# Performance work log

Measured on AMD Instinct MI355X. Metric: run time of the kernel, lower is better.

Reference implementation:

```python
import jax, jax.numpy as jnp
import numpy as np

B, C, T, D = 4, 64, 256, 256   # batch, channel, time, in_feat
H, DK, OUT = 4, 64, 256        # heads, d_k, out_feat
MIN_VALUE = float(np.finfo(np.float32).min)


def _complex_linear(xr, xi, wr, wi, br, bi):
    # ComplexLinear: (fc_r(xr) - fc_i(xi), fc_r(xi) + fc_i(xr))
    out_r = (xr @ wr + br) - (xi @ wi + bi)
    out_i = (xi @ wr + br) + (xr @ wi + bi)
    return out_r, out_i


def setup_inputs() -> dict:
    key = jax.random.key(0)
    ks = jax.random.split(key, 23)
    s = 1.0 / np.sqrt(D)
    inp = {}
    names = ['q_r', 'q_i', 'k_r', 'k_i', 'v_r', 'v_i']
    for i, n in enumerate(names):
        inp[n] = jax.random.normal(ks[i], (B, C, T, D), dtype=jnp.float32)
    inp['mask'] = jnp.ones((B, 1, C), dtype=jnp.int32)
    pi = 6
    for proj in ['q', 'k', 'v', 'o']:
        out_dim = OUT if proj == 'o' else D
        inp[f'w{proj}_r'] = jax.random.normal(ks[pi], (D, out_dim), dtype=jnp.float32) * s; pi += 1
        inp[f'w{proj}_i'] = jax.random.normal(ks[pi], (D, out_dim), dtype=jnp.float32) * s; pi += 1
        inp[f'b{proj}_r'] = jax.random.normal(ks[pi], (out_dim,), dtype=jnp.float32) * 0.01; pi += 1
        inp[f'b{proj}_i'] = jax.random.normal(ks[pi], (out_dim,), dtype=jnp.float32) * 0.01; pi += 1
    return inp


def _split_heads(x):
    # (B, C, T, D) -> (B, H, T, C, DK)  [view + transpose(1,3)]
    return x.reshape(B, C, T, H, DK).transpose(0, 3, 2, 1, 4)


def _attention(q_r, q_i, k_r, k_i, v_r, v_i, mask,
               wq_r, wq_i, bq_r, bq_i, wk_r, wk_i, bk_r, bk_i,
               wv_r, wv_i, bv_r, bv_i, wo_r, wo_i, bo_r, bo_i):
    qr, qi = _complex_linear(q_r, q_i, wq_r, wq_i, bq_r, bq_i)
    kr, ki = _complex_linear(k_r, k_i, wk_r, wk_i, bk_r, bk_i)
    vr, vi = _complex_linear(v_r, v_i, wv_r, wv_i, bv_r, bv_i)
    qr, qi, kr, ki, vr, vi = map(_split_heads, (qr, qi, kr, ki, vr, vi))

    # scores = conj(q) @ k^T  (conjugate_transpose_matmul_conjugate), scaled by 1/sqrt(d_k)
    scale = 1.0 / np.sqrt(DK)
    s_r = (jnp.einsum('bhtcd,bhted->bhtce', qr, kr)
           + jnp.einsum('bhtcd,bhted->bhtce', qi, ki)) * scale
    s_i = (jnp.einsum('bhtcd,bhted->bhtce', qr, ki)
           - jnp.einsum('bhtcd,bhted->bhtce', qi, kr)) * scale

    # amplitude softmax with masking (mask: (B,1,C) -> (B,1,1,1,C), eq(0))
    mask_b = (mask == 0)[:, None, None]  # (B,1,1,1,C)
    amp = jnp.sqrt(s_r * s_r + s_i * s_i)
    amp = jnp.where(mask_b, MIN_VALUE, amp)
    sc = jax.nn.softmax(amp, axis=-1) / amp
    a_r = jnp.where(mask_b, 0.0, sc * s_r)
    a_i = jnp.where(mask_b, 0.0, sc * s_i)

    # complex matmul attn @ v
    x_r = (jnp.einsum('bhtce,bhted->bhtcd', a_r, vr)
           - jnp.einsum('bhtce,bhted->bhtcd', a_i, vi))
    x_i = (jnp.einsum('bhtce,bhted->bhtcd', a_i, vr)
           + jnp.einsum('bhtce,bhted->bhtcd', a_r, vi))

    # (B,H,T,C,DK) -> (B,C,T,H*DK)
    x_r = x_r.transpose(0, 3, 2, 1, 4).reshape(B, C, T, H * DK)
    x_i = x_i.transpose(0, 3, 2, 1, 4).reshape(B, C, T, H * DK)
    return _complex_linear(x_r, x_i, wo_r, wo_i, bo_r, bo_i)


def reference(q_r, q_i, k_r, k_i, v_r, v_i, mask,
              wq_r, wq_i, bq_r, bq_i, wk_r, wk_i, bk_r, bk_i,
              wv_r, wv_i, bv_r, bv_i, wo_r, wo_i, bo_r, bo_i):
    return _attention(q_r, q_i, k_r, k_i, v_r, v_i, mask,
                      wq_r, wq_i, bq_r, bq_i, wk_r, wk_i, bk_r, bk_i,
                      wv_r, wv_i, bv_r, bv_i, wo_r, wo_i, bo_r, bo_i)
```

## Files before the change

### kernel.cpp

```cpp
#include <hip/hip_runtime.h>
#include <hip/hip_bf16.h>
#include <cstddef>

#define MIN_VALUE_F (-3.402823466e38f)


typedef __attribute__((ext_vector_type(8))) __bf16 bfrag;
typedef __attribute__((ext_vector_type(4))) float f32x4;

__device__ __forceinline__ float bf2f(unsigned int u) {
    union { unsigned int i; float f; } v; v.i = u << 16; return v.f;
}
__device__ __forceinline__ unsigned short f2bf(float f) {
    union { float f; unsigned int i; } v; v.f = f;
    return (unsigned short)((v.i + 0x7fffu + ((v.i >> 16) & 1u)) >> 16);
}
__device__ __forceinline__ unsigned int cvt2(float a, float b) {
    __hip_bfloat16 lo = __float2bfloat16(a);
    __hip_bfloat16 hi = __float2bfloat16(b);
    union { __hip_bfloat16 h[2]; unsigned int u; } x;
    x.h[0] = lo; x.h[1] = hi;
    return x.u;
}
__device__ __forceinline__ bfrag negf(bfrag v) {
    union { bfrag b; unsigned int u[4]; } x; x.b = v;
    #pragma unroll
    for (int i = 0; i < 4; ++i) x.u[i] ^= 0x80008000u;
    return x.b;
}

typedef __attribute__((address_space(3))) void lds_void_t;
typedef const __attribute__((address_space(1))) void gmem_void_t;
__device__ __forceinline__ void glds16(const void* g, void* l) {
    __builtin_amdgcn_global_load_lds((gmem_void_t*)g, (lds_void_t*)l, 16, 0, 0);
}

__device__ __forceinline__ bfrag rdfrag(const unsigned short* arr, int row, int slot) {
    const int s = slot ^ (row & 7);
    return *(const bfrag*)&arr[row * 64 + s * 8];
}

__global__ __launch_bounds__(256)
void wprep_kernel(const float* __restrict__ w0, const float* __restrict__ w1,
                  const float* __restrict__ w2, const float* __restrict__ w3,
                  const float* __restrict__ w4, const float* __restrict__ w5,
                  unsigned short* __restrict__ dst)
{
    const int my = blockIdx.y;
    const float* wsrc[6] = {w0, w1, w2, w3, w4, w5};
    const float* w = wsrc[my];
    const int cid = blockIdx.x * 256 + threadIdx.x;
    const int ss = cid & 3;
    const int n  = (cid >> 2) & 63;
    const int s  = (cid >> 8) & 7;
    const int nt = (cid >> 11) & 3;
    const int nn = nt * 64 + n;
    const int kb = s * 32 + ((ss ^ ((n >> 1) & 3)) << 3);
    unsigned int p[4];
    #pragma unroll
    for (int jj = 0; jj < 4; ++jj) {
        const float a = w[(size_t)(kb + 2 * jj) * 256 + nn];
        const float b = w[(size_t)(kb + 2 * jj + 1) * 256 + nn];
        p[jj] = cvt2(a, b);
    }
    uint4 q; q.x = p[0]; q.y = p[1]; q.z = p[2]; q.w = p[3];
    *(uint4*)&dst[(size_t)my * 65536 + (size_t)cid * 8] = q;
}

__global__ __launch_bounds__(256, 4)
void proj_mfma(const float* __restrict__ xq_r, const float* __restrict__ xq_i,
               const float* __restrict__ xk_r, const float* __restrict__ xk_i,
               const float* __restrict__ xv_r, const float* __restrict__ xv_i,
               const unsigned short* __restrict__ wimg,
               const float* __restrict__ bq_r, const float* __restrict__ bq_i,
               const float* __restrict__ bk_r, const float* __restrict__ bk_i,
               const float* __restrict__ bv_r, const float* __restrict__ bv_i,
               unsigned short* __restrict__ ws_out)
{
    __shared__ __align__(16) unsigned short SH[8192];

    const int pz = blockIdx.z;
    const float *xr, *xi, *br_, *bi_;
    if (pz == 0)      { xr = xq_r; xi = xq_i; br_ = bq_r; bi_ = bq_i; }
    else if (pz == 1) { xr = xk_r; xi = xk_i; br_ = bk_r; bi_ = bk_i; }
    else              { xr = xv_r; xi = xv_i; br_ = bv_r; bi_ = bv_i; }
    unsigned short* outr = ws_out + (size_t)pz * 2 * 16777216;
    unsigned short* outi = outr + 16777216;

    const int tid = threadIdx.x;
    const int lane = tid & 63, wv = tid >> 6;
    const int l15 = lane & 15, hi = lane >> 4;
    const int wm = (wv >> 1) * 32, wn = (wv & 1) * 32;
    const int ny = blockIdx.x;
    const int m0 = blockIdx.y * 64;

    const unsigned short* wr_img = wimg + (size_t)pz * 131072 + ny * 16384;
    const unsigned short* wi_img = wr_img + 65536;

    unsigned short* As_r = SH;
    unsigned short* As_i = SH + 2048;
    unsigned short* Ws_r = SH + 4096;
    unsigned short* Ws_i = SH + 6144;

    const int arow = tid >> 2;
    const int apos = tid & 3;
    const int asw = apos ^ ((arow >> 1) & 3);
    const int aidx = arow * 32 + (asw << 3);
    float4 fr0, fr1, fi0, fi1;
    uint4 wbr, wbi;

    f32x4 accR[2][2] = {}, accI[2][2] = {};

    auto load_step = [&](int s) {
        const size_t o = (size_t)(m0 + arow) * 256 + s * 32 + apos * 8;
        fr0 = *(const float4*)(xr + o);
        fr1 = *(const float4*)(xr + o + 4);
        fi0 = *(const float4*)(xi + o);
        fi1 = *(const float4*)(xi + o + 4);
        wbr = *(const uint4*)(wr_img + s * 2048 + tid * 8);
        wbi = *(const uint4*)(wi_img + s * 2048 + tid * 8);
    };
    auto write_stage = [&]() {
        uint4 p, q;
        p.x = cvt2(fr0.x, fr0.y); p.y = cvt2(fr0.z, fr0.w);
        p.z = cvt2(fr1.x, fr1.y); p.w = cvt2(fr1.z, fr1.w);
        q.x = cvt2(fi0.x, fi0.y); q.y = cvt2(fi0.z, fi0.w);
        q.z = cvt2(fi1.x, fi1.y); q.w = cvt2(fi1.z, fi1.w);
        *(uint4*)&As_r[aidx] = p;
        *(uint4*)&As_i[aidx] = q;
        *(uint4*)&Ws_r[tid * 8] = wbr;
        *(uint4*)&Ws_i[tid * 8] = wbi;
    };

    load_step(0);
    write_stage();
    __syncthreads();

    for (int s = 0; s < 8; ++s) {
        if (s < 7) load_step(s + 1);
        bfrag ar[2], ai[2], nai[2];
        #pragma unroll
        for (int mf = 0; mf < 2; ++mf) {
            const int m = wm + mf * 16 + l15;
            const int idx = m * 32 + ((hi ^ ((m >> 1) & 3)) << 3);
            ar[mf] = *(const bfrag*)&As_r[idx];
            ai[mf] = *(const bfrag*)&As_i[idx];
            nai[mf] = negf(ai[mf]);
        }
        #pragma unroll
        for (int nf = 0; nf < 2; ++nf) {
            const int n = wn + nf * 16 + l15;
            const int idx = n * 32 + ((hi ^ ((n >> 1) & 3)) << 3);
            const bfrag brf = *(const bfrag*)&Ws_r[idx];
            const bfrag bif = *(const bfrag*)&Ws_i[idx];
            #pragma unroll
            for (int mf = 0; mf < 2; ++mf) {
                accR[mf][nf] = __builtin_amdgcn_mfma_f32_16x16x32_bf16(ar[mf], brf, accR[mf][nf], 0, 0, 0);
                accR[mf][nf] = __builtin_amdgcn_mfma_f32_16x16x32_bf16(nai[mf], bif, accR[mf][nf], 0, 0, 0);
                accI[mf][nf] = __builtin_amdgcn_mfma_f32_16x16x32_bf16(ai[mf], brf, accI[mf][nf], 0, 0, 0);
                accI[mf][nf] = __builtin_amdgcn_mfma_f32_16x16x32_bf16(ar[mf], bif, accI[mf][nf], 0, 0, 0);
            }
        }
        __syncthreads();
        if (s < 7) { write_stage(); __syncthreads(); }
    }

    const int bc = m0 >> 8, b = bc >> 6, c = bc & 63, t0 = m0 & 255;
    #pragma unroll
    for (int nf = 0; nf < 2; ++nf) {
        const int n_loc = wn + nf * 16 + l15;
        const int n_glob = ny * 64 + n_loc;
        const float vbr = br_[n_glob], vbi = bi_[n_glob];
        const float addR = vbr - vbi, addI = vbr + vbi;
        #pragma unroll
        for (int mf = 0; mf < 2; ++mf) {
            #pragma unroll
            for (int r = 0; r < 4; ++r) {
                const int m_loc = wm + mf * 16 + hi * 4 + r;
                SH[m_loc * 64 + n_loc] = f2bf(accR[mf][nf][r] + addR);
                SH[4096 + m_loc * 64 + n_loc] = f2bf(accI[mf][nf][r] + addI);
            }
        }
    }
    __syncthreads();
    const int h = ny;
    #pragma unroll
    for (int p = 0; p < 2; ++p) {
        const int tr = (tid >> 3) + p * 32;
        const int dk = (tid & 7) * 8;
        const int L = tr * 64 + dk;
        const size_t g = (((size_t)(b * 4 + h) * 256 + (t0 + tr)) * 64 + c) * 64 + dk;
        *(uint4*)&outr[g] = *(const uint4*)&SH[L];
        *(uint4*)&outi[g] = *(const uint4*)&SH[4096 + L];
    }
}

__global__ __launch_bounds__(256)
void attn_mfma(const unsigned short* __restrict__ Qg_r, const unsigned short* __restrict__ Qg_i,
               const unsigned short* __restrict__ Kg_r, const unsigned short* __restrict__ Kg_i,
               const unsigned short* __restrict__ Vg_r, const unsigned short* __restrict__ Vg_i,
               const int* __restrict__ mask,
               unsigned short* __restrict__ Xr, unsigned short* __restrict__ Xi)
{
    __shared__ __align__(16) unsigned short sQr[4096], sQi[4096];
    __shared__ __align__(16) unsigned short sKr[4096], sKi[4096];
    __shared__ __align__(16) unsigned short sVr[4608], sVi[4608];
    __shared__ int smask[64];

    const int bht = blockIdx.x;
    const int b = bht >> 10;
    const int h = (bht >> 8) & 3;
    const int t = bht & 255;
    const size_t base = (size_t)bht * 4096;
    const int tid = threadIdx.x;
    const int lane = tid & 63, wv = tid >> 6;
    const int l15 = lane & 15, hi = lane >> 4;

    const int ep = (lane & 31) * 2;
    const int dch = wv * 2 + (lane >> 5);
    const unsigned short* vr0p = Vg_r + base + (size_t)ep * 64 + dch * 8;
    const unsigned short* vi0p = Vg_i + base + (size_t)ep * 64 + dch * 8;
    const uint4 vr0 = *(const uint4*)vr0p;
    const uint4 vr1 = *(const uint4*)(vr0p + 64);
    const uint4 vi0 = *(const uint4*)vi0p;
    const uint4 vi1 = *(const uint4*)(vi0p + 64);

    #pragma unroll
    for (int i = 0; i < 2; ++i) {
        const int ch = wv * 128 + i * 64 + lane;
        const int r = ch >> 3, cg = ch & 7;
        const int so = r * 64 + ((cg ^ (r & 7)) << 3);
        const int dofs = (wv * 128 + i * 64) << 3;
        glds16(Qg_r + base + so, &sQr[dofs]);
        glds16(Qg_i + base + so, &sQi[dofs]);
        glds16(Kg_r + base + so, &sKr[dofs]);
        glds16(Kg_i + base + so, &sKi[dofs]);
    }
    if (tid < 64) smask[tid] = mask[b * 64 + tid];

    {
        union { uint4 v; unsigned short s[8]; } ar0, ar1, ai0, ai1;
        ar0.v = vr0; ar1.v = vr1; ai0.v = vi0; ai1.v = vi1;
        #pragma unroll
        for (int j = 0; j < 8; ++j) {
            const int d = dch * 8 + j;
            *(unsigned int*)&sVr[d * 72 + ep] = (unsigned)ar0.s[j] | ((unsigned)ar1.s[j] << 16);
            *(unsigned int*)&sVi[d * 72 + ep] = (unsigned)ai0.s[j] | ((unsigned)ai1.s[j] << 16);
        }
    }
    __syncthreads();

    const int cq = wv * 16 + l15;
    f32x4 aR[4] = {}, aI[4] = {};
    #pragma unroll
    for (int ks = 0; ks < 2; ++ks) {
        const int slot = ks * 4 + hi;
        const bfrag qr = rdfrag(sQr, cq, slot);
        const bfrag qi = rdfrag(sQi, cq, slot);
        const bfrag nqi = negf(qi);
        #pragma unroll
        for (int et = 0; et < 4; ++et) {
            const int re = et * 16 + l15;
            const bfrag kr = rdfrag(sKr, re, slot);
            const bfrag ki = rdfrag(sKi, re, slot);
            aR[et] = __builtin_amdgcn_mfma_f32_16x16x32_bf16(kr, qr, aR[et], 0, 0, 0);
            aR[et] = __builtin_amdgcn_mfma_f32_16x16x32_bf16(ki, qi, aR[et], 0, 0, 0);
            aI[et] = __builtin_amdgcn_mfma_f32_16x16x32_bf16(ki, qr, aI[et], 0, 0, 0);
            aI[et] = __builtin_amdgcn_mfma_f32_16x16x32_bf16(kr, nqi, aI[et], 0, 0, 0);
        }
    }
    __syncthreads();

    const float scale = 0.125f;
    float amp[4][4], ex[4][4];
    float mx = MIN_VALUE_F;
    #pragma unroll
    for (int et = 0; et < 4; ++et) {
        #pragma unroll
        for (int r = 0; r < 4; ++r) {
            const float sr = aR[et][r] * scale;
            const float si = aI[et][r] * scale;
            float a = sqrtf(fmaf(sr, sr, si * si));
            if (smask[et * 16 + hi * 4 + r] == 0) a = MIN_VALUE_F;
            amp[et][r] = a;
            mx = fmaxf(mx, a);
        }
    }
    mx = fmaxf(mx, __shfl_xor(mx, 16, 64));
    mx = fmaxf(mx, __shfl_xor(mx, 32, 64));
    float sm = 0.f;
    #pragma unroll
    for (int et = 0; et < 4; ++et) {
        #pragma unroll
        for (int r = 0; r < 4; ++r) {
            const float e_ = expf(amp[et][r] - mx);
            ex[et][r] = e_; sm += e_;
        }
    }
    sm += __shfl_xor(sm, 16, 64);
    sm += __shfl_xor(sm, 32, 64);

    #pragma unroll
    for (int et = 0; et < 4; ++et) {
        float pr[4], pi[4];
        #pragma unroll
        for (int r = 0; r < 4; ++r) {
            const float w = ex[et][r] * __builtin_amdgcn_rcpf(sm * amp[et][r]);
            pr[r] = w * (aR[et][r] * scale);
            pi[r] = w * (aI[et][r] * scale);
        }
        const int pidx = cq * 64 + ((et * 16 + hi * 4) ^ ((cq & 7) << 3));
        uint2 ur, ui;
        ur.x = cvt2(pr[0], pr[1]); ur.y = cvt2(pr[2], pr[3]);
        ui.x = cvt2(pi[0], pi[1]); ui.y = cvt2(pi[2], pi[3]);
        *(uint2*)&sQr[pidx] = ur;
        *(uint2*)&sQi[pidx] = ui;
    }
    __syncthreads();

    f32x4 xR4[4] = {}, xI4[4] = {};
    #pragma unroll
    for (int ks = 0; ks < 2; ++ks) {
        const int slot = ks * 4 + hi;
        const bfrag pr = rdfrag(sQr, cq, slot);
        const bfrag pi = rdfrag(sQi, cq, slot);
        const bfrag npi = negf(pi);
        #pragma unroll
        for (int dt = 0; dt < 4; ++dt) {
            const int rd = dt * 16 + l15;
            const bfrag vr = *(const bfrag*)&sVr[rd * 72 + ks * 32 + hi * 8];
            const bfrag vi = *(const bfrag*)&sVi[rd * 72 + ks * 32 + hi * 8];
            xR4[dt] = __builtin_amdgcn_mfma_f32_16x16x32_bf16(pr, vr, xR4[dt], 0, 0, 0);
            xR4[dt] = __builtin_amdgcn_mfma_f32_16x16x32_bf16(npi, vi, xR4[dt], 0, 0, 0);
            xI4[dt] = __builtin_amdgcn_mfma_f32_16x16x32_bf16(pi, vr, xI4[dt], 0, 0, 0);
            xI4[dt] = __builtin_amdgcn_mfma_f32_16x16x32_bf16(pr, vi, xI4[dt], 0, 0, 0);
        }
    }

    #pragma unroll
    for (int dt = 0; dt < 4; ++dt) {
        #pragma unroll
        for (int r = 0; r < 4; ++r) {
            const int c = wv * 16 + hi * 4 + r;
            const size_t o = (((size_t)(b * 64 + c) * 256) + t) * 256 + h * 64 + dt * 16 + l15;
            Xr[o] = f2bf(xR4[dt][r]);
            Xi[o] = f2bf(xI4[dt][r]);
        }
    }
}

__global__ __launch_bounds__(256, 4)
void oproj_mfma(const unsigned short* __restrict__ Xr_g, const unsigned short* __restrict__ Xi_g,
                const unsigned short* __restrict__ wimg,
                const float* __restrict__ bo_r, const float* __restrict__ bo_i,
                float* __restrict__ outr, float* __restrict__ outi)
{
    __shared__ __align__(16) unsigned short SH[8192];

    const int tid = threadIdx.x;
    const int lane = tid & 63, wv = tid >> 6;
    const int l15 = lane & 15, hi = lane >> 4;
    const int wm = (wv >> 1) * 32, wn = (wv & 1) * 32;
    const int ny = blockIdx.x;
    const int m0 = blockIdx.y * 64;

    const unsigned short* wr_img = wimg + ny * 16384;
    const unsigned short* wi_img = wr_img + 65536;

    unsigned short* As_r = SH;
    unsigned short* As_i = SH + 2048;
    unsigned short* Ws_r = SH + 4096;
    unsigned short* Ws_i = SH + 6144;

    const int xrow = tid >> 2;
    const int xslot = tid & 3;
    const int xsw = xslot ^ ((xrow >> 1) & 3);
    const int xidx = xrow * 32 + xslot * 8;
    uint4 xbr, xbi, wbr, wbi;

    f32x4 accR[2][2] = {}, accI[2][2] = {};

    auto load_step = [&](int s) {
        const size_t o = (size_t)(m0 + xrow) * 256 + s * 32 + xsw * 8;
        xbr = *(const uint4*)(Xr_g + o);
        xbi = *(const uint4*)(Xi_g + o);
        wbr = *(const uint4*)(wr_img + s * 2048 + tid * 8);
        wbi = *(const uint4*)(wi_img + s * 2048 + tid * 8);
    };
    auto write_stage = [&]() {
        *(uint4*)&As_r[xidx] = xbr;
        *(uint4*)&As_i[xidx] = xbi;
        *(uint4*)&Ws_r[tid * 8] = wbr;
        *(uint4*)&Ws_i[tid * 8] = wbi;
    };

    load_step(0);
    write_stage();
    __syncthreads();

    for (int s = 0; s < 8; ++s) {
        if (s < 7) load_step(s + 1);
        bfrag ar[2], ai[2], nai[2];
        #pragma unroll
        for (int mf = 0; mf < 2; ++mf) {
            const int m = wm + mf * 16 + l15;
            const int idx = m * 32 + ((hi ^ ((m >> 1) & 3)) << 3);
            ar[mf] = *(const bfrag*)&As_r[idx];
            ai[mf] = *(const bfrag*)&As_i[idx];
            nai[mf] = negf(ai[mf]);
        }
        #pragma unroll
        for (int nf = 0; nf < 2; ++nf) {
            const int n = wn + nf * 16 + l15;
            const int idx = n * 32 + ((hi ^ ((n >> 1) & 3)) << 3);
            const bfrag brf = *(const bfrag*)&Ws_r[idx];
            const bfrag bif = *(const bfrag*)&Ws_i[idx];
            #pragma unroll
            for (int mf = 0; mf < 2; ++mf) {
                accR[mf][nf] = __builtin_amdgcn_mfma_f32_16x16x32_bf16(ar[mf], brf, accR[mf][nf], 0, 0, 0);
                accR[mf][nf] = __builtin_amdgcn_mfma_f32_16x16x32_bf16(nai[mf], bif, accR[mf][nf], 0, 0, 0);
                accI[mf][nf] = __builtin_amdgcn_mfma_f32_16x16x32_bf16(ai[mf], brf, accI[mf][nf], 0, 0, 0);
                accI[mf][nf] = __builtin_amdgcn_mfma_f32_16x16x32_bf16(ar[mf], bif, accI[mf][nf], 0, 0, 0);
            }
        }
        __syncthreads();
        if (s < 7) { write_stage(); __syncthreads(); }
    }

    #pragma unroll
    for (int nf = 0; nf < 2; ++nf) {
        const int n = ny * 64 + wn + nf * 16 + l15;
        const float vbr = bo_r[n], vbi = bo_i[n];
        const float addR = vbr - vbi, addI = vbr + vbi;
        #pragma unroll
        for (int mf = 0; mf < 2; ++mf) {
            #pragma unroll
            for (int r = 0; r < 4; ++r) {
                const size_t o = (size_t)(m0 + wm + mf * 16 + hi * 4 + r) * 256 + n;
                outr[o] = accR[mf][nf][r] + addR;
                outi[o] = accI[mf][nf][r] + addI;
            }
        }
    }
}

extern "C" void kernel_launch(void* const* d_in, const int* in_sizes, int n_in,
                              void* d_out, int out_size, void* d_ws, size_t ws_size,
                              hipStream_t stream)
{
    (void)in_sizes; (void)n_in; (void)out_size; (void)ws_size;
    const float* q_r = (const float*)d_in[0];
    const float* q_i = (const float*)d_in[1];
    const float* k_r = (const float*)d_in[2];
    const float* k_i = (const float*)d_in[3];
    const float* v_r = (const float*)d_in[4];
    const float* v_i = (const float*)d_in[5];
    const int* mask = (const int*)d_in[6];
    const float* wq_r = (const float*)d_in[7];
    const float* wq_i = (const float*)d_in[8];
    const float* bq_r = (const float*)d_in[9];
    const float* bq_i = (const float*)d_in[10];
    const float* wk_r = (const float*)d_in[11];
    const float* wk_i = (const float*)d_in[12];
    const float* bk_r = (const float*)d_in[13];
    const float* bk_i = (const float*)d_in[14];
    const float* wv_r = (const float*)d_in[15];
    const float* wv_i = (const float*)d_in[16];
    const float* bv_r = (const float*)d_in[17];
    const float* bv_i = (const float*)d_in[18];
    const float* wo_r = (const float*)d_in[19];
    const float* wo_i = (const float*)d_in[20];
    const float* bo_r = (const float*)d_in[21];
    const float* bo_i = (const float*)d_in[22];

    const size_t TS = 16777216;
    unsigned short* ws = (unsigned short*)d_ws;
    unsigned short* Q = ws;
    unsigned short* Xr = ws + 6 * TS;
    unsigned short* Xi = ws + 7 * TS;
    unsigned short* wimg_qkv = ws + 6 * TS;
    unsigned short* wimg_o = ws;

    wprep_kernel<<<dim3(32, 6), 256, 0, stream>>>(wq_r, wq_i, wk_r, wk_i, wv_r, wv_i, wimg_qkv);
    proj_mfma<<<dim3(4, 1024, 3), 256, 0, stream>>>(q_r, q_i, k_r, k_i, v_r, v_i, wimg_qkv,
                                                    bq_r, bq_i, bk_r, bk_i, bv_r, bv_i, ws);
    attn_mfma<<<dim3(4096), 256, 0, stream>>>(Q, Q + TS, Q + 2 * TS, Q + 3 * TS,
                                              Q + 4 * TS, Q + 5 * TS, mask, Xr, Xi);
    wprep_kernel<<<dim3(32, 2), 256, 0, stream>>>(wo_r, wo_i, wo_r, wo_r, wo_r, wo_r, wimg_o);
    oproj_mfma<<<dim3(4, 1024), 256, 0, stream>>>(Xr, Xi, wimg_o, bo_r, bo_i,
                                                  (float*)d_out, (float*)d_out + TS);
}
```

Before: 392.2 us.

## Double-buffer LDS stages and remap blocks for XCD-local tile reuse in projections

Projection and output-projection GEMM kernels now use two LDS buffers so the next k-slice is written while the current one is consumed, removing one barrier per step. Launches are flattened to 1D with a block-id remap that keeps the four column tiles of each row block on the same XCD, so activation rows can be reused from the shared L2 instead of being refetched. This doubles LDS per block, which may reduce occupancy.

```diff
diff --git a/kernel.cpp b/kernel.cpp
--- a/kernel.cpp
+++ b/kernel.cpp
@@ -77,9 +77,15 @@
                const float* __restrict__ bv_r, const float* __restrict__ bv_i,
                unsigned short* __restrict__ ws_out)
 {
-    __shared__ __align__(16) unsigned short SH[8192];
-
-    const int pz = blockIdx.z;
+    __shared__ __align__(16) unsigned short SH[16384];
+
+    const int bid = blockIdx.x;
+    const int work = (bid & 7) * 1536 + (bid >> 3);
+    const int ny = work & 3;
+    const int rest = work >> 2;
+    const int m0 = (rest & 1023) * 64;
+    const int pz = rest >> 10;
+
     const float *xr, *xi, *br_, *bi_;
     if (pz == 0)      { xr = xq_r; xi = xq_i; br_ = bq_r; bi_ = bq_i; }
     else if (pz == 1) { xr = xk_r; xi = xk_i; br_ = bk_r; bi_ = bk_i; }
@@ -91,16 +97,9 @@
     const int lane = tid & 63, wv = tid >> 6;
     const int l15 = lane & 15, hi = lane >> 4;
     const int wm = (wv >> 1) * 32, wn = (wv & 1) * 32;
-    const int ny = blockIdx.x;
-    const int m0 = blockIdx.y * 64;
 
     const unsigned short* wr_img = wimg + (size_t)pz * 131072 + ny * 16384;
     const unsigned short* wi_img = wr_img + 65536;
-
-    unsigned short* As_r = SH;
-    unsigned short* As_i = SH + 2048;
-    unsigned short* Ws_r = SH + 4096;
-    unsigned short* Ws_i = SH + 6144;
 
     const int arow = tid >> 2;
     const int apos = tid & 3;
@@ -120,24 +119,30 @@
         wbr = *(const uint4*)(wr_img + s * 2048 + tid * 8);
         wbi = *(const uint4*)(wi_img + s * 2048 + tid * 8);
     };
-    auto write_stage = [&]() {
+    auto write_stage = [&](int buf) {
+        unsigned short* B = SH + buf * 8192;
         uint4 p, q;
         p.x = cvt2(fr0.x, fr0.y); p.y = cvt2(fr0.z, fr0.w);
         p.z = cvt2(fr1.x, fr1.y); p.w = cvt2(fr1.z, fr1.w);
         q.x = cvt2(fi0.x, fi0.y); q.y = cvt2(fi0.z, fi0.w);
         q.z = cvt2(fi1.x, fi1.y); q.w = cvt2(fi1.z, fi1.w);
-        *(uint4*)&As_r[aidx] = p;
-        *(uint4*)&As_i[aidx] = q;
-        *(uint4*)&Ws_r[tid * 8] = wbr;
-        *(uint4*)&Ws_i[tid * 8] = wbi;
+        *(uint4*)&B[aidx] = p;
+        *(uint4*)&B[2048 + aidx] = q;
+        *(uint4*)&B[4096 + tid * 8] = wbr;
+        *(uint4*)&B[6144 + tid * 8] = wbi;
     };
 
     load_step(0);
-    write_stage();
+    write_stage(0);
     __syncthreads();
 
     for (int s = 0; s < 8; ++s) {
+        const int b = s & 1;
         if (s < 7) load_step(s + 1);
+        const unsigned short* As_r = SH + b * 8192;
+        const unsigned short* As_i = As_r + 2048;
+        const unsigned short* Ws_r = As_r + 4096;
+        const unsigned short* Ws_i = As_r + 6144;
         bfrag ar[2], ai[2], nai[2];
         #pragma unroll
         for (int mf = 0; mf < 2; ++mf) {
@@ -161,8 +166,8 @@
                 accI[mf][nf] = __builtin_amdgcn_mfma_f32_16x16x32_bf16(ar[mf], bif, accI[mf][nf], 0, 0, 0);
             }
         }
+        if (s < 7) write_stage(b ^ 1);
         __syncthreads();
-        if (s < 7) { write_stage(); __syncthreads(); }
     }
 
     const int bc = m0 >> 8, b = bc >> 6, c = bc & 63, t0 = m0 & 255;
@@ -355,22 +360,20 @@
                 const float* __restrict__ bo_r, const float* __restrict__ bo_i,
                 float* __restrict__ outr, float* __restrict__ outi)
 {
-    __shared__ __align__(16) unsigned short SH[8192];
+    __shared__ __align__(16) unsigned short SH[16384];
+
+    const int bid = blockIdx.x;
+    const int work = (bid & 7) * 512 + (bid >> 3);
+    const int ny = work & 3;
+    const int m0 = (work >> 2) * 64;
 
     const int tid = threadIdx.x;
     const int lane = tid & 63, wv = tid >> 6;
     const int l15 = lane & 15, hi = lane >> 4;
     const int wm = (wv >> 1) * 32, wn = (wv & 1) * 32;
-    const int ny = blockIdx.x;
-    const int m0 = blockIdx.y * 64;
 
     const unsigned short* wr_img = wimg + ny * 16384;
     const unsigned short* wi_img = wr_img + 65536;
-
-    unsigned short* As_r = SH;
-    unsigned short* As_i = SH + 2048;
-    unsigned short* Ws_r = SH + 4096;
-    unsigned short* Ws_i = SH + 6144;
 
     const int xrow = tid >> 2;
     const int xslot = tid & 3;
@@ -387,19 +390,25 @@
         wbr = *(const uint4*)(wr_img + s * 2048 + tid * 8);
         wbi = *(const uint4*)(wi_img + s * 2048 + tid * 8);
     };
-    auto write_stage = [&]() {
-        *(uint4*)&As_r[xidx] = xbr;
-        *(uint4*)&As_i[xidx] = xbi;
-        *(uint4*)&Ws_r[tid * 8] = wbr;
-        *(uint4*)&Ws_i[tid * 8] = wbi;
+    auto write_stage = [&](int buf) {
+        unsigned short* B = SH + buf * 8192;
+        *(uint4*)&B[xidx] = xbr;
+        *(uint4*)&B[2048 + xidx] = xbi;
+        *(uint4*)&B[4096 + tid * 8] = wbr;
+        *(uint4*)&B[6144 + tid * 8] = wbi;
     };
 
     load_step(0);
-    write_stage();
+    write_stage(0);
     __syncthreads();
 
     for (int s = 0; s < 8; ++s) {
+        const int b = s & 1;
         if (s < 7) load_step(s + 1);
+        const unsigned short* As_r = SH + b * 8192;
+        const unsigned short* As_i = As_r + 2048;
+        const unsigned short* Ws_r = As_r + 4096;
+        const unsigned short* Ws_i = As_r + 6144;
         bfrag ar[2], ai[2], nai[2];
         #pragma unroll
         for (int mf = 0; mf < 2; ++mf) {
@@ -423,8 +432,8 @@
                 accI[mf][nf] = __builtin_amdgcn_mfma_f32_16x16x32_bf16(ar[mf], bif, accI[mf][nf], 0, 0, 0);
             }
         }
+        if (s < 7) write_stage(b ^ 1);
         __syncthreads();
-        if (s < 7) { write_stage(); __syncthreads(); }
     }
 
     #pragma unroll
@@ -482,11 +491,11 @@
     unsigned short* wimg_o = ws;
 
     wprep_kernel<<<dim3(32, 6), 256, 0, stream>>>(wq_r, wq_i, wk_r, wk_i, wv_r, wv_i, wimg_qkv);
-    proj_mfma<<<dim3(4, 1024, 3), 256, 0, stream>>>(q_r, q_i, k_r, k_i, v_r, v_i, wimg_qkv,
-                                                    bq_r, bq_i, bk_r, bk_i, bv_r, bv_i, ws);
+    proj_mfma<<<dim3(12288), 256, 0, stream>>>(q_r, q_i, k_r, k_i, v_r, v_i, wimg_qkv,
+                                               bq_r, bq_i, bk_r, bk_i, bv_r, bv_i, ws);
     attn_mfma<<<dim3(4096), 256, 0, stream>>>(Q, Q + TS, Q + 2 * TS, Q + 3 * TS,
                                               Q + 4 * TS, Q + 5 * TS, mask, Xr, Xi);
     wprep_kernel<<<dim3(32, 2), 256, 0, stream>>>(wo_r, wo_i, wo_r, wo_r, wo_r, wo_r, wimg_o);
-    oproj_mfma<<<dim3(4, 1024), 256, 0, stream>>>(Xr, Xi, wimg_o, bo_r, bo_i,
-                                                  (float*)d_out, (float*)d_out + TS);
-}
+    oproj_mfma<<<dim3(4096), 256, 0, stream>>>(Xr, Xi, wimg_o, bo_r, bo_i,
+                                               (float*)d_out, (float*)d_out + TS);
+}
```

New measurement: 332.2 us, median of 2. 15.3% less time.
